# Optimization experiments

Hardware: AMD Instinct MI355X
Metric: run time of the kernel (lower is better)

The kernel has to match this reference:

```python
import jax, jax.numpy as jnp
import numpy as np

T, K, E, D, F = 2048, 6, 32, 2048, 1408   # tokens, top_k, routed experts, dim, moe_inter_dim
S = 2                                      # fused shared experts
C = T * K // E                             # exact per-expert capacity (balanced routing)


def _silu_and_mul(gu):
    # merged gate_up activation: silu(gate_half) * up_half
    g, u = jnp.split(gu, 2, axis=-1)
    return jax.nn.silu(g) * u


def setup_inputs() -> dict:
    key = jax.random.key(0)
    ks = jax.random.split(key, 7)
    x = jax.random.normal(ks[0], (T, D), dtype=jnp.float32)
    # balanced routing: every expert receives exactly C = T*K/E token-expert pairs
    indices = jax.random.permutation(ks[1], jnp.arange(T * K, dtype=jnp.int32) % E).reshape(T, K)
    weights = jax.random.uniform(ks[2], (T, K), dtype=jnp.float32)
    scale = 0.02
    w_gate_up = jax.random.normal(ks[3], (E, D, 2 * F), dtype=jnp.float32) * scale
    w_down = jax.random.normal(ks[4], (E, F, D), dtype=jnp.float32) * scale
    w_gate_up_shared = jax.random.normal(ks[5], (S, D, 2 * F), dtype=jnp.float32) * scale
    w_down_shared = jax.random.normal(ks[6], (S, F, D), dtype=jnp.float32) * scale
    return {"x": x, "weights": weights, "w_gate_up": w_gate_up, "w_down": w_down,
            "w_gate_up_shared": w_gate_up_shared, "w_down_shared": w_down_shared,
            "indices": indices}


def reference(x, weights, w_gate_up, w_down, w_gate_up_shared, w_down_shared, indices):
    # ---- dispatch: sort token-expert pairs by expert id (balanced -> exactly C per expert)
    flat_e = indices.reshape(-1)                       # [T*K]
    order = jnp.argsort(flat_e, stable=True)           # [T*K] pair ids grouped by expert
    tok = order // K                                   # source token of each sorted pair
    w_sorted = weights.reshape(-1)[order]              # routing weight of each sorted pair
    xg = x[tok].reshape(E, C, D)                       # gathered per-expert inputs
    # ---- routed experts: grouped gate_up GEMM -> silu_and_mul -> down GEMM
    act = _silu_and_mul(jnp.einsum('ecd,edf->ecf', xg, w_gate_up))   # [E, C, F]
    down = jnp.einsum('ecf,efd->ecd', act, w_down)                   # [E, C, D]
    # ---- combine: weighted scatter-add back to token order (y[idx] += out * weights[idx, top])
    y = jnp.zeros_like(x).at[tok].add(down.reshape(E * C, D) * w_sorted[:, None])
    # ---- fused shared experts: run on all tokens, added unweighted
    act_s = _silu_and_mul(jnp.einsum('td,sdf->stf', x, w_gate_up_shared))  # [S, T, F]
    y = y + jnp.einsum('stf,sfd->td', act_s, w_down_shared)
    return y
```

## Files before the change

kernel.cpp:

```cpp
#include <hip/hip_runtime.h>
#include <hip/hip_bf16.h>

#define TT 2048
#define KK 6
#define EE 32
#define DD 2048
#define FF 1408
#define SS 2
#define CC 384

typedef __bf16 bf16_t;
typedef __attribute__((ext_vector_type(8))) __bf16 bf16x8;
typedef __attribute__((ext_vector_type(4))) float f32x4;
typedef unsigned int u32;

#define AS1 __attribute__((address_space(1)))
#define AS3 __attribute__((address_space(3)))

__device__ __forceinline__ u32 f2bf(float f) {
    u32 u = __builtin_bit_cast(u32, f);
    return (u + 0x7fffu + ((u >> 16) & 1u)) >> 16;
}
__device__ __forceinline__ u32 pack2(float a, float b) {
    return f2bf(a) | (f2bf(b) << 16);
}
__device__ __forceinline__ float silu_mul(float g, float u) {
    return (g / (1.0f + __expf(-g))) * u;
}

__global__ void k_dispatch(const int* __restrict__ idx, int* __restrict__ counts,
                           int* __restrict__ tok, int* __restrict__ sop) {
    int p = blockIdx.x * 256 + threadIdx.x;
    if (p >= TT * KK) return;
    int e = idx[p];
    int pos = atomicAdd(&counts[e], 1);
    int slot = e * CC + pos;
    tok[slot] = p / KK;
    sop[p] = slot;
}

__global__ void k_gather(const float* __restrict__ x, const int* __restrict__ tok,
                         bf16_t* __restrict__ xall) {
    int row = blockIdx.x;
    int srow = (row < EE * CC) ? tok[row] : (row - EE * CC);
    const float* src = x + (size_t)srow * DD;
    bf16_t* dst = xall + (size_t)row * DD;
    int c0 = threadIdx.x * 8;
    float4 a = *(const float4*)(src + c0);
    float4 b = *(const float4*)(src + c0 + 4);
    uint4 o;
    o.x = pack2(a.x, a.y); o.y = pack2(a.z, a.w);
    o.z = pack2(b.x, b.y); o.w = pack2(b.z, b.w);
    *(uint4*)(dst + c0) = o;
}

#define BSTR 40

template<bool FUSED>
__global__ __launch_bounds__(512) void k_gemm_r(
    const bf16_t* __restrict__ Aall, const float* __restrict__ Br,
    bf16_t* __restrict__ Out, int Kdim, int Bstr, int Ostr, int NB)
{
    const int lin = blockIdx.x;
    const int xcd = lin & 7, jj = lin >> 3;
    const int e = xcd + 8 * (jj / NB);
    const int nblk = jj % NB;

    const bf16_t* A = Aall + (size_t)e * CC * Kdim;
    const float* Bbase = Br + (size_t)e * Kdim * Bstr;

    const int tid = threadIdx.x;
    const int lane = tid & 63, wid = tid >> 6;
    const int m_base = (wid >> 1) * 96, wn = wid & 1;
    const int l15 = lane & 15, lq = lane >> 4;
    const int arow = tid >> 2, ac = tid & 3;
    const int bn = tid & 127, kb = (tid >> 7) * 8;

    const float* bsrc;
    bf16_t* Cout;
    if (FUSED) {
        bsrc = Bbase + ((bn & 64) ? FF : 0) + nblk * 64 + (bn & 63);
        Cout = Out + (size_t)e * CC * Ostr + nblk * 64;
    } else {
        bsrc = Bbase + nblk * 128 + bn;
        Cout = Out + (size_t)e * CC * Ostr + nblk * 128;
    }

    __shared__ __align__(16) bf16_t As[3][384 * 32];
    __shared__ __align__(16) bf16_t Bs[2][128 * BSTR];

    f32x4 acc[6][4] = {};
    const int ksteps = Kdim >> 5;

    auto stageA = [&](int kt, bf16_t* dst) {
        const int k0 = kt << 5;
        #pragma unroll
        for (int i = 0; i < 3; ++i) {
            const int row = i * 128 + arow;
            const int cs = ac ^ ((row >> 1) & 3);
            const bf16_t* g = A + (size_t)row * Kdim + (k0 + cs * 8);
            AS3 u32* l = (AS3 u32*)(void*)(dst + (size_t)(i * 128 + wid * 16) * 32);
            __builtin_amdgcn_global_load_lds((const AS1 u32*)(const void*)g, l, 16, 0, 0);
        }
    };
    auto loadB = [&](int kt, float* v) {
        const float* sp = bsrc + (size_t)((kt << 5) + kb) * Bstr;
        #pragma unroll
        for (int t = 0; t < 8; ++t) v[t] = sp[(size_t)t * Bstr];
    };
    auto writeB = [&](bf16_t* bbuf, const float* v) {
        uint4 w;
        w.x = pack2(v[0], v[1]); w.y = pack2(v[2], v[3]);
        w.z = pack2(v[4], v[5]); w.w = pack2(v[6], v[7]);
        *(uint4*)(bbuf + (size_t)bn * BSTR + kb) = w;
    };
    auto compute = [&](const bf16_t* abuf, const bf16_t* bbuf) {
        bf16x8 bfr[4];
        #pragma unroll
        for (int j = 0; j < 4; ++j) {
            const int n_ds = FUSED ? (wn * 32 + (j & 1) * 16 + (j >> 1) * 64)
                                   : (wn * 64 + j * 16);
            bfr[j] = *(const bf16x8*)(bbuf + (size_t)(n_ds + l15) * BSTR + lq * 8);
        }
        #pragma unroll
        for (int m = 0; m < 6; ++m) {
            const int row = m_base + m * 16 + l15;
            bf16x8 af = *(const bf16x8*)(abuf + (size_t)row * 32 + (size_t)((lq ^ ((row >> 1) & 3)) * 8));
            #pragma unroll
            for (int j = 0; j < 4; ++j)
                acc[m][j] = __builtin_amdgcn_mfma_f32_16x16x32_bf16(af, bfr[j], acc[m][j], 0, 0, 0);
        }
    };

    float vBa[8], vBb[8];
    bf16_t *aR = &As[0][0], *aS = &As[1][0], *aT = &As[2][0];

    loadB(0, vBa);
    stageA(0, aR);
    asm volatile("s_waitcnt vmcnt(3)" ::: "memory");
    writeB(&Bs[0][0], vBa);
    loadB(1, vBb);
    stageA(1, aS);
    asm volatile("s_waitcnt lgkmcnt(0)" ::: "memory");
    __builtin_amdgcn_s_barrier();

    for (int t = 0; t < ksteps - 2; t += 2) {
        loadB(t + 2, vBa);
        asm volatile("s_waitcnt vmcnt(19)" ::: "memory");
        asm volatile("s_waitcnt lgkmcnt(0)" ::: "memory");
        __builtin_amdgcn_s_barrier();
        stageA(t + 2, aT);
        compute(aR, &Bs[0][0]);
        asm volatile("s_waitcnt vmcnt(14)" ::: "memory");
        writeB(&Bs[1][0], vBb);
        { bf16_t* tmp = aR; aR = aS; aS = aT; aT = tmp; }
        loadB(t + 3, vBb);
        asm volatile("s_waitcnt vmcnt(19)" ::: "memory");
        asm volatile("s_waitcnt lgkmcnt(0)" ::: "memory");
        __builtin_amdgcn_s_barrier();
        stageA(t + 3, aT);
        compute(aR, &Bs[1][0]);
        asm volatile("s_waitcnt vmcnt(14)" ::: "memory");
        writeB(&Bs[0][0], vBa);
        { bf16_t* tmp = aR; aR = aS; aS = aT; aT = tmp; }
    }

    asm volatile("s_waitcnt vmcnt(11)" ::: "memory");
    asm volatile("s_waitcnt lgkmcnt(0)" ::: "memory");
    __builtin_amdgcn_s_barrier();
    compute(aR, &Bs[0][0]);
    asm volatile("s_waitcnt vmcnt(3)" ::: "memory");
    writeB(&Bs[1][0], vBb);
    asm volatile("s_waitcnt vmcnt(0)" ::: "memory");
    asm volatile("s_waitcnt lgkmcnt(0)" ::: "memory");
    __builtin_amdgcn_s_barrier();
    compute(aS, &Bs[1][0]);

    if (FUSED) {
        #pragma unroll
        for (int m = 0; m < 6; ++m)
            #pragma unroll
            for (int j = 0; j < 2; ++j) {
                const int n = wn * 32 + j * 16 + l15;
                #pragma unroll
                for (int r = 0; r < 4; ++r) {
                    const int mm = m_base + m * 16 + lq * 4 + r;
                    Cout[(size_t)mm * Ostr + n] = (bf16_t)silu_mul(acc[m][j][r], acc[m][j + 2][r]);
                }
            }
    } else {
        #pragma unroll
        for (int m = 0; m < 6; ++m)
            #pragma unroll
            for (int j = 0; j < 4; ++j) {
                const int n = wn * 64 + j * 16 + l15;
                #pragma unroll
                for (int r = 0; r < 4; ++r) {
                    const int mm = m_base + m * 16 + lq * 4 + r;
                    Cout[(size_t)mm * Ostr + n] = (bf16_t)acc[m][j][r];
                }
            }
    }
}

template<bool FUSED>
__global__ __launch_bounds__(256) void k_gemm_s(
    const bf16_t* __restrict__ Ash, const float* __restrict__ Bsh,
    bf16_t* __restrict__ Out, int Kdim, int Bstr, int Ostr, int ash_stride,
    int nkeys, int KQ, int NBs)
{
    const int b = blockIdx.x;
    const int xcd = b & 7, jj = b >> 3;
    const int m = jj / KQ, kq = jj % KQ;
    const int key = kq * 8 + xcd;
    if (key >= nkeys) return;
    const int s = key / NBs, nb = key % NBs;

    const bf16_t* A = Ash + ((size_t)s * ash_stride + (size_t)m * 128) * Kdim;
    const float* Bp = Bsh + (size_t)s * Kdim * Bstr;

    const int tid = threadIdx.x;
    const int lane = tid & 63, wid = tid >> 6;
    const int m_off = (wid >> 1) * 64, wn = wid & 1;
    const int l15 = lane & 15, lq = lane >> 4;
    const int arow = tid >> 2, ac = tid & 3;
    const int bn = tid & 127, kb = (tid >> 7) * 16;

    const float* bsrc;
    bf16_t* Cout;
    if (FUSED) {
        bsrc = Bp + (((tid >> 6) & 1) ? FF : 0) + nb * 64 + (tid & 63);
        Cout = Out + ((size_t)s * TT + (size_t)m * 128) * Ostr + nb * 64;
    } else {
        bsrc = Bp + nb * 128 + bn;
        Cout = Out + ((size_t)s * TT + (size_t)m * 128) * Ostr + nb * 128;
    }

    __shared__ __align__(16) bf16_t As[3][128 * 32];
    __shared__ __align__(16) bf16_t Bs[2][128 * BSTR];

    f32x4 acc[4][4] = {};
    const int ksteps = Kdim >> 5;

    auto stageA = [&](int kt, bf16_t* dst) {
        const int k0 = kt << 5;
        #pragma unroll
        for (int i = 0; i < 2; ++i) {
            const int row = i * 64 + arow;
            const int cs = ac ^ ((row >> 1) & 3);
            const bf16_t* g = A + (size_t)row * Kdim + (k0 + cs * 8);
            AS3 u32* l = (AS3 u32*)(void*)(dst + (size_t)(i * 64 + wid * 16) * 32);
            __builtin_amdgcn_global_load_lds((const AS1 u32*)(const void*)g, l, 16, 0, 0);
        }
    };
    auto loadB = [&](int kt, float* v) {
        const float* sp = bsrc + (size_t)((kt << 5) + kb) * Bstr;
        #pragma unroll
        for (int t = 0; t < 16; ++t) v[t] = sp[(size_t)t * Bstr];
    };
    auto writeB = [&](bf16_t* bbuf, const float* v) {
        u32 p[8];
        #pragma unroll
        for (int t = 0; t < 8; ++t) p[t] = pack2(v[2 * t], v[2 * t + 1]);
        uint4 w0, w1;
        w0.x = p[0]; w0.y = p[1]; w0.z = p[2]; w0.w = p[3];
        w1.x = p[4]; w1.y = p[5]; w1.z = p[6]; w1.w = p[7];
        *(uint4*)(bbuf + (size_t)bn * BSTR + kb) = w0;
        *(uint4*)(bbuf + (size_t)bn * BSTR + kb + 8) = w1;
    };
    auto compute = [&](const bf16_t* abuf, const bf16_t* bbuf) {
        bf16x8 af[4], bfr[4];
        #pragma unroll
        for (int i = 0; i < 4; ++i) {
            const int row = m_off + i * 16 + l15;
            af[i] = *(const bf16x8*)(abuf + (size_t)row * 32 + (size_t)((lq ^ ((row >> 1) & 3)) * 8));
        }
        #pragma unroll
        for (int j = 0; j < 4; ++j) {
            const int n_ds = FUSED ? (wn * 32 + (j & 1) * 16 + (j >> 1) * 64)
                                   : (wn * 64 + j * 16);
            bfr[j] = *(const bf16x8*)(bbuf + (size_t)(n_ds + l15) * BSTR + lq * 8);
        }
        #pragma unroll
        for (int i = 0; i < 4; ++i)
            #pragma unroll
            for (int j = 0; j < 4; ++j)
                acc[i][j] = __builtin_amdgcn_mfma_f32_16x16x32_bf16(af[i], bfr[j], acc[i][j], 0, 0, 0);
    };

    float vBa[16], vBb[16];
    bf16_t *aR = &As[0][0], *aS = &As[1][0], *aT = &As[2][0];

    loadB(0, vBa);
    stageA(0, aR);
    asm volatile("s_waitcnt vmcnt(2)" ::: "memory");
    writeB(&Bs[0][0], vBa);
    loadB(1, vBb);
    stageA(1, aS);
    asm volatile("s_waitcnt lgkmcnt(0)" ::: "memory");
    __builtin_amdgcn_s_barrier();

    for (int t = 0; t < ksteps - 2; t += 2) {
        loadB(t + 2, vBa);
        asm volatile("s_waitcnt vmcnt(34)" ::: "memory");
        asm volatile("s_waitcnt lgkmcnt(0)" ::: "memory");
        __builtin_amdgcn_s_barrier();
        stageA(t + 2, aT);
        compute(aR, &Bs[0][0]);
        asm volatile("s_waitcnt vmcnt(20)" ::: "memory");
        writeB(&Bs[1][0], vBb);
        { bf16_t* tmp = aR; aR = aS; aS = aT; aT = tmp; }
        loadB(t + 3, vBb);
        asm volatile("s_waitcnt vmcnt(34)" ::: "memory");
        asm volatile("s_waitcnt lgkmcnt(0)" ::: "memory");
        __builtin_amdgcn_s_barrier();
        stageA(t + 3, aT);
        compute(aR, &Bs[1][0]);
        asm volatile("s_waitcnt vmcnt(20)" ::: "memory");
        writeB(&Bs[0][0], vBa);
        { bf16_t* tmp = aR; aR = aS; aS = aT; aT = tmp; }
    }

    asm volatile("s_waitcnt vmcnt(18)" ::: "memory");
    asm volatile("s_waitcnt lgkmcnt(0)" ::: "memory");
    __builtin_amdgcn_s_barrier();
    compute(aR, &Bs[0][0]);
    asm volatile("s_waitcnt vmcnt(2)" ::: "memory");
    writeB(&Bs[1][0], vBb);
    asm volatile("s_waitcnt vmcnt(0)" ::: "memory");
    asm volatile("s_waitcnt lgkmcnt(0)" ::: "memory");
    __builtin_amdgcn_s_barrier();
    compute(aS, &Bs[1][0]);

    if (FUSED) {
        #pragma unroll
        for (int i = 0; i < 4; ++i)
            #pragma unroll
            for (int j = 0; j < 2; ++j) {
                const int n = wn * 32 + j * 16 + l15;
                #pragma unroll
                for (int r = 0; r < 4; ++r) {
                    const int mm = m_off + i * 16 + lq * 4 + r;
                    Cout[(size_t)mm * Ostr + n] = (bf16_t)silu_mul(acc[i][j][r], acc[i][j + 2][r]);
                }
            }
    } else {
        #pragma unroll
        for (int i = 0; i < 4; ++i)
            #pragma unroll
            for (int j = 0; j < 4; ++j) {
                const int n = wn * 64 + j * 16 + l15;
                #pragma unroll
                for (int r = 0; r < 4; ++r) {
                    const int mm = m_off + i * 16 + lq * 4 + r;
                    Cout[(size_t)mm * Ostr + n] = (bf16_t)acc[i][j][r];
                }
            }
    }
}

__global__ void k_combine(const bf16_t* __restrict__ down, const int* __restrict__ sop,
                          const float* __restrict__ wts, float* __restrict__ y) {
    int t = blockIdx.x;
    int d0 = threadIdx.x * 8;
    float a[8] = {0, 0, 0, 0, 0, 0, 0, 0};
    #pragma unroll
    for (int k = 0; k < KK; ++k) {
        int slot = sop[t * KK + k];
        float w = wts[t * KK + k];
        bf16x8 v = *(const bf16x8*)(down + (size_t)slot * DD + d0);
        #pragma unroll
        for (int j = 0; j < 8; ++j) a[j] += w * (float)v[j];
    }
    #pragma unroll
    for (int s = 0; s < SS; ++s) {
        bf16x8 v = *(const bf16x8*)(down + ((size_t)EE * CC + (size_t)s * TT + t) * DD + d0);
        #pragma unroll
        for (int j = 0; j < 8; ++j) a[j] += (float)v[j];
    }
    float4 o0, o1;
    o0.x = a[0]; o0.y = a[1]; o0.z = a[2]; o0.w = a[3];
    o1.x = a[4]; o1.y = a[5]; o1.z = a[6]; o1.w = a[7];
    *(float4*)(y + (size_t)t * DD + d0) = o0;
    *(float4*)(y + (size_t)t * DD + d0 + 4) = o1;
}

extern "C" void kernel_launch(void* const* d_in, const int* in_sizes, int n_in,
                              void* d_out, int out_size, void* d_ws, size_t ws_size,
                              hipStream_t stream) {
    (void)in_sizes; (void)n_in; (void)out_size; (void)ws_size;
    const float* x      = (const float*)d_in[0];
    const float* wts    = (const float*)d_in[1];
    const float* w_gu   = (const float*)d_in[2];
    const float* w_dn   = (const float*)d_in[3];
    const float* w_gu_s = (const float*)d_in[4];
    const float* w_dn_s = (const float*)d_in[5];
    const int*   indices= (const int*)d_in[6];
    float* y = (float*)d_out;

    char* ws = (char*)d_ws;
    size_t off = 0;
    auto alloc = [&](size_t bytes) {
        void* p = ws + off;
        off = (off + bytes + 255) & ~(size_t)255;
        return p;
    };
    int*    counts = (int*)alloc((size_t)EE * 4);
    int*    tok    = (int*)alloc((size_t)EE * CC * 4);
    int*    sop    = (int*)alloc((size_t)TT * KK * 4);
    bf16_t* xall   = (bf16_t*)alloc((size_t)(EE * CC + TT) * DD * 2);
    bf16_t* actb   = (bf16_t*)alloc((size_t)(EE * CC + SS * TT) * FF * 2);
    bf16_t* dnout  = (bf16_t*)alloc((size_t)(EE * CC + SS * TT) * DD * 2);

    hipMemsetAsync(counts, 0, EE * 4, stream);
    k_dispatch<<<(TT * KK + 255) / 256, 256, 0, stream>>>(indices, counts, tok, sop);
    k_gather<<<EE * CC + TT, 256, 0, stream>>>(x, tok, xall);

    k_gemm_r<true><<<EE * 22, 512, 0, stream>>>(xall, w_gu, actb, DD, 2 * FF, FF, 22);
    k_gemm_s<true><<<8 * 6 * 16, 256, 0, stream>>>(
        xall + (size_t)EE * CC * DD, w_gu_s, actb + (size_t)EE * CC * FF,
        DD, 2 * FF, FF, 0, 44, 6, 22);

    k_gemm_r<false><<<EE * 16, 512, 0, stream>>>(actb, w_dn, dnout, FF, DD, DD, 16);
    k_gemm_s<false><<<8 * 4 * 16, 256, 0, stream>>>(
        actb + (size_t)EE * CC * FF, w_dn_s, dnout + (size_t)EE * CC * DD,
        FF, DD, DD, TT, 32, 4, 16);

    k_combine<<<TT, 256, 0, stream>>>(dnout, sop, wts, y);
}
```

Baseline: 1.485 ms.

## Double routed GEMM K-tile to 64 with two-stage A buffering and setprio

```diff
diff --git a/kernel.cpp b/kernel.cpp
--- a/kernel.cpp
+++ b/kernel.cpp
@@ -54,8 +54,6 @@
     *(uint4*)(dst + c0) = o;
 }
 
-#define BSTR 40
-
 template<bool FUSED>
 __global__ __launch_bounds__(512) void k_gemm_r(
     const bf16_t* __restrict__ Aall, const float* __restrict__ Br,
@@ -73,8 +71,8 @@
     const int lane = tid & 63, wid = tid >> 6;
     const int m_base = (wid >> 1) * 96, wn = wid & 1;
     const int l15 = lane & 15, lq = lane >> 4;
-    const int arow = tid >> 2, ac = tid & 3;
-    const int bn = tid & 127, kb = (tid >> 7) * 8;
+    const int arow8 = tid >> 3, achunk = tid & 7;
+    const int bn = tid & 127, kb = (tid >> 7) * 16;
 
     const float* bsrc;
     bf16_t* Cout;
@@ -86,95 +84,98 @@
         Cout = Out + (size_t)e * CC * Ostr + nblk * 128;
     }
 
-    __shared__ __align__(16) bf16_t As[3][384 * 32];
-    __shared__ __align__(16) bf16_t Bs[2][128 * BSTR];
+    __shared__ __align__(16) bf16_t As[2][384 * 64];
+    __shared__ __align__(16) bf16_t Bs[2][128 * 72];
 
     f32x4 acc[6][4] = {};
-    const int ksteps = Kdim >> 5;
+    const int ks = Kdim >> 6;
 
     auto stageA = [&](int kt, bf16_t* dst) {
-        const int k0 = kt << 5;
-        #pragma unroll
-        for (int i = 0; i < 3; ++i) {
-            const int row = i * 128 + arow;
-            const int cs = ac ^ ((row >> 1) & 3);
-            const bf16_t* g = A + (size_t)row * Kdim + (k0 + cs * 8);
-            AS3 u32* l = (AS3 u32*)(void*)(dst + (size_t)(i * 128 + wid * 16) * 32);
+        const int k0 = kt << 6;
+        #pragma unroll
+        for (int i = 0; i < 6; ++i) {
+            const int row = i * 64 + arow8;
+            const int c = achunk ^ (row & 7);
+            const bf16_t* g = A + (size_t)row * Kdim + (k0 + c * 8);
+            AS3 u32* l = (AS3 u32*)(void*)(dst + (size_t)(i * 64 + wid * 8) * 64);
             __builtin_amdgcn_global_load_lds((const AS1 u32*)(const void*)g, l, 16, 0, 0);
         }
     };
     auto loadB = [&](int kt, float* v) {
-        const float* sp = bsrc + (size_t)((kt << 5) + kb) * Bstr;
-        #pragma unroll
-        for (int t = 0; t < 8; ++t) v[t] = sp[(size_t)t * Bstr];
+        const float* sp = bsrc + (size_t)((kt << 6) + kb) * Bstr;
+        #pragma unroll
+        for (int t = 0; t < 16; ++t) v[t] = sp[(size_t)t * Bstr];
     };
     auto writeB = [&](bf16_t* bbuf, const float* v) {
-        uint4 w;
-        w.x = pack2(v[0], v[1]); w.y = pack2(v[2], v[3]);
-        w.z = pack2(v[4], v[5]); w.w = pack2(v[6], v[7]);
-        *(uint4*)(bbuf + (size_t)bn * BSTR + kb) = w;
+        uint4 w0, w1;
+        w0.x = pack2(v[0], v[1]);   w0.y = pack2(v[2], v[3]);
+        w0.z = pack2(v[4], v[5]);   w0.w = pack2(v[6], v[7]);
+        w1.x = pack2(v[8], v[9]);   w1.y = pack2(v[10], v[11]);
+        w1.z = pack2(v[12], v[13]); w1.w = pack2(v[14], v[15]);
+        *(uint4*)(bbuf + (size_t)bn * 72 + kb) = w0;
+        *(uint4*)(bbuf + (size_t)bn * 72 + kb + 8) = w1;
     };
     auto compute = [&](const bf16_t* abuf, const bf16_t* bbuf) {
-        bf16x8 bfr[4];
-        #pragma unroll
-        for (int j = 0; j < 4; ++j) {
-            const int n_ds = FUSED ? (wn * 32 + (j & 1) * 16 + (j >> 1) * 64)
-                                   : (wn * 64 + j * 16);
-            bfr[j] = *(const bf16x8*)(bbuf + (size_t)(n_ds + l15) * BSTR + lq * 8);
+        __builtin_amdgcn_s_setprio(1);
+        #pragma unroll
+        for (int kh = 0; kh < 2; ++kh) {
+            bf16x8 bfr[4];
+            #pragma unroll
+            for (int j = 0; j < 4; ++j) {
+                const int n_ds = FUSED ? (wn * 32 + (j & 1) * 16 + (j >> 1) * 64)
+                                       : (wn * 64 + j * 16);
+                bfr[j] = *(const bf16x8*)(bbuf + (size_t)(n_ds + l15) * 72 + kh * 32 + lq * 8);
+            }
+            #pragma unroll
+            for (int m = 0; m < 6; ++m) {
+                const int row = m_base + m * 16 + l15;
+                bf16x8 af = *(const bf16x8*)(abuf + (size_t)row * 64
+                               + (size_t)(((kh * 4 + lq) ^ (row & 7)) * 8));
+                #pragma unroll
+                for (int j = 0; j < 4; ++j)
+                    acc[m][j] = __builtin_amdgcn_mfma_f32_16x16x32_bf16(af, bfr[j], acc[m][j], 0, 0, 0);
+            }
         }
-        #pragma unroll
-        for (int m = 0; m < 6; ++m) {
-            const int row = m_base + m * 16 + l15;
-            bf16x8 af = *(const bf16x8*)(abuf + (size_t)row * 32 + (size_t)((lq ^ ((row >> 1) & 3)) * 8));
-            #pragma unroll
-            for (int j = 0; j < 4; ++j)
-                acc[m][j] = __builtin_amdgcn_mfma_f32_16x16x32_bf16(af, bfr[j], acc[m][j], 0, 0, 0);
-        }
-    };
-
-    float vBa[8], vBb[8];
-    bf16_t *aR = &As[0][0], *aS = &As[1][0], *aT = &As[2][0];
+        __builtin_amdgcn_s_setprio(0);
+    };
+
+    float vBa[16], vBb[16];
 
     loadB(0, vBa);
-    stageA(0, aR);
-    asm volatile("s_waitcnt vmcnt(3)" ::: "memory");
+    asm volatile("s_waitcnt vmcnt(0)" ::: "memory");
     writeB(&Bs[0][0], vBa);
     loadB(1, vBb);
-    stageA(1, aS);
-    asm volatile("s_waitcnt lgkmcnt(0)" ::: "memory");
-    __builtin_amdgcn_s_barrier();
-
-    for (int t = 0; t < ksteps - 2; t += 2) {
+    stageA(0, &As[0][0]);
+    asm volatile("s_waitcnt lgkmcnt(0)" ::: "memory");
+    __builtin_amdgcn_s_barrier();
+
+    for (int t = 0; t < ks - 2; t += 2) {
         loadB(t + 2, vBa);
-        asm volatile("s_waitcnt vmcnt(19)" ::: "memory");
+        asm volatile("s_waitcnt vmcnt(16)" ::: "memory");
         asm volatile("s_waitcnt lgkmcnt(0)" ::: "memory");
         __builtin_amdgcn_s_barrier();
-        stageA(t + 2, aT);
-        compute(aR, &Bs[0][0]);
-        asm volatile("s_waitcnt vmcnt(14)" ::: "memory");
+        stageA(t + 1, &As[1][0]);
+        compute(&As[0][0], &Bs[0][0]);
         writeB(&Bs[1][0], vBb);
-        { bf16_t* tmp = aR; aR = aS; aS = aT; aT = tmp; }
         loadB(t + 3, vBb);
-        asm volatile("s_waitcnt vmcnt(19)" ::: "memory");
+        asm volatile("s_waitcnt vmcnt(16)" ::: "memory");
         asm volatile("s_waitcnt lgkmcnt(0)" ::: "memory");
         __builtin_amdgcn_s_barrier();
-        stageA(t + 3, aT);
-        compute(aR, &Bs[1][0]);
-        asm volatile("s_waitcnt vmcnt(14)" ::: "memory");
+        stageA(t + 2, &As[0][0]);
+        compute(&As[1][0], &Bs[1][0]);
         writeB(&Bs[0][0], vBa);
-        { bf16_t* tmp = aR; aR = aS; aS = aT; aT = tmp; }
-    }
-
-    asm volatile("s_waitcnt vmcnt(11)" ::: "memory");
-    asm volatile("s_waitcnt lgkmcnt(0)" ::: "memory");
-    __builtin_amdgcn_s_barrier();
-    compute(aR, &Bs[0][0]);
-    asm volatile("s_waitcnt vmcnt(3)" ::: "memory");
+    }
+
+    asm volatile("s_waitcnt vmcnt(0)" ::: "memory");
+    asm volatile("s_waitcnt lgkmcnt(0)" ::: "memory");
+    __builtin_amdgcn_s_barrier();
+    stageA(ks - 1, &As[1][0]);
+    compute(&As[0][0], &Bs[0][0]);
     writeB(&Bs[1][0], vBb);
     asm volatile("s_waitcnt vmcnt(0)" ::: "memory");
     asm volatile("s_waitcnt lgkmcnt(0)" ::: "memory");
     __builtin_amdgcn_s_barrier();
-    compute(aS, &Bs[1][0]);
+    compute(&As[1][0], &Bs[1][0]);
 
     if (FUSED) {
         #pragma unroll
@@ -203,6 +204,7 @@
     }
 }
 
+#define BSTR 40
 template<bool FUSED>
 __global__ __launch_bounds__(256) void k_gemm_s(
     const bf16_t* __restrict__ Ash, const float* __restrict__ Bsh,
```

Measured after the change: 1.490 ms. About the same (+0.4%).

## Rework GEMM pipelines to deep B register prefetch with double-buffered A

Applied to the files above, without the earlier changes.

```diff
diff --git a/kernel.cpp b/kernel.cpp
--- a/kernel.cpp
+++ b/kernel.cpp
@@ -74,7 +74,7 @@
     const int m_base = (wid >> 1) * 96, wn = wid & 1;
     const int l15 = lane & 15, lq = lane >> 4;
     const int arow = tid >> 2, ac = tid & 3;
-    const int bn = tid & 127, kb = (tid >> 7) * 8;
+    const int bn = tid & 127, kq = tid >> 7;
 
     const float* bsrc;
     bf16_t* Cout;
@@ -86,25 +86,25 @@
         Cout = Out + (size_t)e * CC * Ostr + nblk * 128;
     }
 
-    __shared__ __align__(16) bf16_t As[3][384 * 32];
+    __shared__ __align__(16) bf16_t As[2][384 * 32];
     __shared__ __align__(16) bf16_t Bs[2][128 * BSTR];
 
     f32x4 acc[6][4] = {};
-    const int ksteps = Kdim >> 5;
+    const int ks = Kdim >> 5;
 
     auto stageA = [&](int kt, bf16_t* dst) {
         const int k0 = kt << 5;
         #pragma unroll
         for (int i = 0; i < 3; ++i) {
             const int row = i * 128 + arow;
-            const int cs = ac ^ ((row >> 1) & 3);
-            const bf16_t* g = A + (size_t)row * Kdim + (k0 + cs * 8);
+            const int c = ac ^ (arow & 3);
+            const bf16_t* g = A + (size_t)row * Kdim + (k0 + c * 8);
             AS3 u32* l = (AS3 u32*)(void*)(dst + (size_t)(i * 128 + wid * 16) * 32);
             __builtin_amdgcn_global_load_lds((const AS1 u32*)(const void*)g, l, 16, 0, 0);
         }
     };
     auto loadB = [&](int kt, float* v) {
-        const float* sp = bsrc + (size_t)((kt << 5) + kb) * Bstr;
+        const float* sp = bsrc + (size_t)((kt << 5) + kq * 8) * Bstr;
         #pragma unroll
         for (int t = 0; t < 8; ++t) v[t] = sp[(size_t)t * Bstr];
     };
@@ -112,9 +112,10 @@
         uint4 w;
         w.x = pack2(v[0], v[1]); w.y = pack2(v[2], v[3]);
         w.z = pack2(v[4], v[5]); w.w = pack2(v[6], v[7]);
-        *(uint4*)(bbuf + (size_t)bn * BSTR + kb) = w;
+        *(uint4*)(bbuf + (size_t)bn * BSTR + kq * 8) = w;
     };
     auto compute = [&](const bf16_t* abuf, const bf16_t* bbuf) {
+        __builtin_amdgcn_s_setprio(1);
         bf16x8 bfr[4];
         #pragma unroll
         for (int j = 0; j < 4; ++j) {
@@ -125,56 +126,36 @@
         #pragma unroll
         for (int m = 0; m < 6; ++m) {
             const int row = m_base + m * 16 + l15;
-            bf16x8 af = *(const bf16x8*)(abuf + (size_t)row * 32 + (size_t)((lq ^ ((row >> 1) & 3)) * 8));
+            bf16x8 af = *(const bf16x8*)(abuf + (size_t)row * 32
+                           + (size_t)((lq ^ (row & 3)) * 8));
             #pragma unroll
             for (int j = 0; j < 4; ++j)
                 acc[m][j] = __builtin_amdgcn_mfma_f32_16x16x32_bf16(af, bfr[j], acc[m][j], 0, 0, 0);
         }
-    };
-
-    float vBa[8], vBb[8];
-    bf16_t *aR = &As[0][0], *aS = &As[1][0], *aT = &As[2][0];
-
-    loadB(0, vBa);
-    stageA(0, aR);
-    asm volatile("s_waitcnt vmcnt(3)" ::: "memory");
-    writeB(&Bs[0][0], vBa);
-    loadB(1, vBb);
-    stageA(1, aS);
-    asm volatile("s_waitcnt lgkmcnt(0)" ::: "memory");
-    __builtin_amdgcn_s_barrier();
-
-    for (int t = 0; t < ksteps - 2; t += 2) {
-        loadB(t + 2, vBa);
-        asm volatile("s_waitcnt vmcnt(19)" ::: "memory");
+        __builtin_amdgcn_s_setprio(0);
+    };
+
+    float r[4][8];
+
+    loadB(0, r[0]);
+    asm volatile("s_waitcnt vmcnt(0)" ::: "memory");
+    writeB(&Bs[0][0], r[0]);
+    loadB(1, r[1]);
+    loadB(2, r[2]);
+    stageA(0, &As[0][0]);
+    loadB(3, r[3]);
+
+    for (int t = 0; t < ks; ++t) {
+        asm volatile("s_waitcnt vmcnt(8)" ::: "memory");
         asm volatile("s_waitcnt lgkmcnt(0)" ::: "memory");
         __builtin_amdgcn_s_barrier();
-        stageA(t + 2, aT);
-        compute(aR, &Bs[0][0]);
-        asm volatile("s_waitcnt vmcnt(14)" ::: "memory");
-        writeB(&Bs[1][0], vBb);
-        { bf16_t* tmp = aR; aR = aS; aS = aT; aT = tmp; }
-        loadB(t + 3, vBb);
-        asm volatile("s_waitcnt vmcnt(19)" ::: "memory");
-        asm volatile("s_waitcnt lgkmcnt(0)" ::: "memory");
-        __builtin_amdgcn_s_barrier();
-        stageA(t + 3, aT);
-        compute(aR, &Bs[1][0]);
-        asm volatile("s_waitcnt vmcnt(14)" ::: "memory");
-        writeB(&Bs[0][0], vBa);
-        { bf16_t* tmp = aR; aR = aS; aS = aT; aT = tmp; }
-    }
-
-    asm volatile("s_waitcnt vmcnt(11)" ::: "memory");
-    asm volatile("s_waitcnt lgkmcnt(0)" ::: "memory");
-    __builtin_amdgcn_s_barrier();
-    compute(aR, &Bs[0][0]);
-    asm volatile("s_waitcnt vmcnt(3)" ::: "memory");
-    writeB(&Bs[1][0], vBb);
-    asm volatile("s_waitcnt vmcnt(0)" ::: "memory");
-    asm volatile("s_waitcnt lgkmcnt(0)" ::: "memory");
-    __builtin_amdgcn_s_barrier();
-    compute(aS, &Bs[1][0]);
+        const int tn = (t + 1 < ks) ? t + 1 : ks - 1;
+        const int tb = (t + 4 < ks) ? t + 4 : ks - 1;
+        stageA(tn, &As[(t + 1) & 1][0]);
+        loadB(tb, r[(t + 4) & 3]);
+        compute(&As[t & 1][0], &Bs[t & 1][0]);
+        writeB(&Bs[(t + 1) & 1][0], r[(t + 1) & 3]);
+    }
 
     if (FUSED) {
         #pragma unroll
@@ -183,9 +164,9 @@
             for (int j = 0; j < 2; ++j) {
                 const int n = wn * 32 + j * 16 + l15;
                 #pragma unroll
-                for (int r = 0; r < 4; ++r) {
-                    const int mm = m_base + m * 16 + lq * 4 + r;
-                    Cout[(size_t)mm * Ostr + n] = (bf16_t)silu_mul(acc[m][j][r], acc[m][j + 2][r]);
+                for (int rr = 0; rr < 4; ++rr) {
+                    const int mm = m_base + m * 16 + lq * 4 + rr;
+                    Cout[(size_t)mm * Ostr + n] = (bf16_t)silu_mul(acc[m][j][rr], acc[m][j + 2][rr]);
                 }
             }
     } else {
@@ -195,9 +176,9 @@
             for (int j = 0; j < 4; ++j) {
                 const int n = wn * 64 + j * 16 + l15;
                 #pragma unroll
-                for (int r = 0; r < 4; ++r) {
-                    const int mm = m_base + m * 16 + lq * 4 + r;
-                    Cout[(size_t)mm * Ostr + n] = (bf16_t)acc[m][j][r];
+                for (int rr = 0; rr < 4; ++rr) {
+                    const int mm = m_base + m * 16 + lq * 4 + rr;
+                    Cout[(size_t)mm * Ostr + n] = (bf16_t)acc[m][j][rr];
                 }
             }
     }
@@ -211,8 +192,8 @@
 {
     const int b = blockIdx.x;
     const int xcd = b & 7, jj = b >> 3;
-    const int m = jj / KQ, kq = jj % KQ;
-    const int key = kq * 8 + xcd;
+    const int m = jj / KQ, kqi = jj % KQ;
+    const int key = kqi * 8 + xcd;
     if (key >= nkeys) return;
     const int s = key / NBs, nb = key % NBs;
 
@@ -224,37 +205,37 @@
     const int m_off = (wid >> 1) * 64, wn = wid & 1;
     const int l15 = lane & 15, lq = lane >> 4;
     const int arow = tid >> 2, ac = tid & 3;
-    const int bn = tid & 127, kb = (tid >> 7) * 16;
+    const int bn = tid & 127, kh = tid >> 7;
 
     const float* bsrc;
     bf16_t* Cout;
     if (FUSED) {
-        bsrc = Bp + (((tid >> 6) & 1) ? FF : 0) + nb * 64 + (tid & 63);
+        bsrc = Bp + ((bn & 64) ? FF : 0) + nb * 64 + (bn & 63);
         Cout = Out + ((size_t)s * TT + (size_t)m * 128) * Ostr + nb * 64;
     } else {
         bsrc = Bp + nb * 128 + bn;
         Cout = Out + ((size_t)s * TT + (size_t)m * 128) * Ostr + nb * 128;
     }
 
-    __shared__ __align__(16) bf16_t As[3][128 * 32];
+    __shared__ __align__(16) bf16_t As[2][128 * 32];
     __shared__ __align__(16) bf16_t Bs[2][128 * BSTR];
 
     f32x4 acc[4][4] = {};
-    const int ksteps = Kdim >> 5;
+    const int ks = Kdim >> 5;
 
     auto stageA = [&](int kt, bf16_t* dst) {
         const int k0 = kt << 5;
         #pragma unroll
         for (int i = 0; i < 2; ++i) {
             const int row = i * 64 + arow;
-            const int cs = ac ^ ((row >> 1) & 3);
-            const bf16_t* g = A + (size_t)row * Kdim + (k0 + cs * 8);
+            const int c = ac ^ (arow & 3);
+            const bf16_t* g = A + (size_t)row * Kdim + (k0 + c * 8);
             AS3 u32* l = (AS3 u32*)(void*)(dst + (size_t)(i * 64 + wid * 16) * 32);
             __builtin_amdgcn_global_load_lds((const AS1 u32*)(const void*)g, l, 16, 0, 0);
         }
     };
     auto loadB = [&](int kt, float* v) {
-        const float* sp = bsrc + (size_t)((kt << 5) + kb) * Bstr;
+        const float* sp = bsrc + (size_t)((kt << 5) + kh * 16) * Bstr;
         #pragma unroll
         for (int t = 0; t < 16; ++t) v[t] = sp[(size_t)t * Bstr];
     };
@@ -265,15 +246,16 @@
         uint4 w0, w1;
         w0.x = p[0]; w0.y = p[1]; w0.z = p[2]; w0.w = p[3];
         w1.x = p[4]; w1.y = p[5]; w1.z = p[6]; w1.w = p[7];
-        *(uint4*)(bbuf + (size_t)bn * BSTR + kb) = w0;
-        *(uint4*)(bbuf + (size_t)bn * BSTR + kb + 8) = w1;
+        *(uint4*)(bbuf + (size_t)bn * BSTR + kh * 16) = w0;
+        *(uint4*)(bbuf + (size_t)bn * BSTR + kh * 16 + 8) = w1;
     };
     auto compute = [&](const bf16_t* abuf, const bf16_t* bbuf) {
         bf16x8 af[4], bfr[4];
         #pragma unroll
         for (int i = 0; i < 4; ++i) {
             const int row = m_off + i * 16 + l15;
-            af[i] = *(const bf16x8*)(abuf + (size_t)row * 32 + (size_t)((lq ^ ((row >> 1) & 3)) * 8));
+            af[i] = *(const bf16x8*)(abuf + (size_t)row * 32
+                       + (size_t)((lq ^ (row & 3)) * 8));
         }
         #pragma unroll
         for (int j = 0; j < 4; ++j) {
@@ -288,49 +270,27 @@
                 acc[i][j] = __builtin_amdgcn_mfma_f32_16x16x32_bf16(af[i], bfr[j], acc[i][j], 0, 0, 0);
     };
 
-    float vBa[16], vBb[16];
-    bf16_t *aR = &As[0][0], *aS = &As[1][0], *aT = &As[2][0];
-
-    loadB(0, vBa);
-    stageA(0, aR);
-    asm volatile("s_waitcnt vmcnt(2)" ::: "memory");
-    writeB(&Bs[0][0], vBa);
-    loadB(1, vBb);
-    stageA(1, aS);
-    asm volatile("s_waitcnt lgkmcnt(0)" ::: "memory");
-    __builtin_amdgcn_s_barrier();
-
-    for (int t = 0; t < ksteps - 2; t += 2) {
-        loadB(t + 2, vBa);
-        asm volatile("s_waitcnt vmcnt(34)" ::: "memory");
+    float r[4][16];
+
+    loadB(0, r[0]);
+    asm volatile("s_waitcnt vmcnt(0)" ::: "memory");
+    writeB(&Bs[0][0], r[0]);
+    loadB(1, r[1]);
+    loadB(2, r[2]);
+    stageA(0, &As[0][0]);
+    loadB(3, r[3]);
+
+    for (int t = 0; t < ks; ++t) {
+        asm volatile("s_waitcnt vmcnt(16)" ::: "memory");
         asm volatile("s_waitcnt lgkmcnt(0)" ::: "memory");
         __builtin_amdgcn_s_barrier();
-        stageA(t + 2, aT);
-        compute(aR, &Bs[0][0]);
-        asm volatile("s_waitcnt vmcnt(20)" ::: "memory");
-        writeB(&Bs[1][0], vBb);
-        { bf16_t* tmp = aR; aR = aS; aS = aT; aT = tmp; }
-        loadB(t + 3, vBb);
-        asm volatile("s_waitcnt vmcnt(34)" ::: "memory");
-        asm volatile("s_waitcnt lgkmcnt(0)" ::: "memory");
-        __builtin_amdgcn_s_barrier();
-        stageA(t + 3, aT);
-        compute(aR, &Bs[1][0]);
-        asm volatile("s_waitcnt vmcnt(20)" ::: "memory");
-        writeB(&Bs[0][0], vBa);
-        { bf16_t* tmp = aR; aR = aS; aS = aT; aT = tmp; }
-    }
-
-    asm volatile("s_waitcnt vmcnt(18)" ::: "memory");
-    asm volatile("s_waitcnt lgkmcnt(0)" ::: "memory");
-    __builtin_amdgcn_s_barrier();
-    compute(aR, &Bs[0][0]);
-    asm volatile("s_waitcnt vmcnt(2)" ::: "memory");
-    writeB(&Bs[1][0], vBb);
-    asm volatile("s_waitcnt vmcnt(0)" ::: "memory");
-    asm volatile("s_waitcnt lgkmcnt(0)" ::: "memory");
-    __builtin_amdgcn_s_barrier();
-    compute(aS, &Bs[1][0]);
+        const int tn = (t + 1 < ks) ? t + 1 : ks - 1;
+        const int tb = (t + 4 < ks) ? t + 4 : ks - 1;
+        stageA(tn, &As[(t + 1) & 1][0]);
+        loadB(tb, r[(t + 4) & 3]);
+        compute(&As[t & 1][0], &Bs[t & 1][0]);
+        writeB(&Bs[(t + 1) & 1][0], r[(t + 1) & 3]);
+    }
 
     if (FUSED) {
         #pragma unroll
@@ -339,9 +299,9 @@
             for (int j = 0; j < 2; ++j) {
                 const int n = wn * 32 + j * 16 + l15;
                 #pragma unroll
-                for (int r = 0; r < 4; ++r) {
-                    const int mm = m_off + i * 16 + lq * 4 + r;
-                    Cout[(size_t)mm * Ostr + n] = (bf16_t)silu_mul(acc[i][j][r], acc[i][j + 2][r]);
+                for (int rr = 0; rr < 4; ++rr) {
+                    const int mm = m_off + i * 16 + lq * 4 + rr;
+                    Cout[(size_t)mm * Ostr + n] = (bf16_t)silu_mul(acc[i][j][rr], acc[i][j + 2][rr]);
                 }
             }
     } else {
@@ -351,9 +311,9 @@
             for (int j = 0; j < 4; ++j) {
                 const int n = wn * 64 + j * 16 + l15;
                 #pragma unroll
-                for (int r = 0; r < 4; ++r) {
-                    const int mm = m_off + i * 16 + lq * 4 + r;
-                    Cout[(size_t)mm * Ostr + n] = (bf16_t)acc[i][j][r];
+                for (int rr = 0; rr < 4; ++rr) {
+                    const int mm = m_off + i * 16 + lq * 4 + rr;
+                    Cout[(size_t)mm * Ostr + n] = (bf16_t)acc[i][j][rr];
                 }
             }
     }
```

Measured after the change: 2.662 ms. 1.79x slower.
